# Performance work log

Hardware: AMD Instinct MI355X
Metric: run time of the kernel (lower is better)

## Reference

```python
import jax, jax.numpy as jnp
import numpy as np

NEG_SLOPE = 0.01  # torch F.leaky_relu default
N_USER = 100000
N_ITEM = 100000
N_EDGE = 640000
D = 128
N_LAYERS = 3  # 1 input + num_hidden_layers(1) + 1 output layer


def setup_inputs() -> dict:
    key = jax.random.key(0)
    ks = jax.random.split(key, 10)
    scale = 1.0 / np.sqrt(D)
    return {
        "h_user": jax.random.normal(ks[0], (N_USER, D), dtype=jnp.float32),
        "h_item": jax.random.normal(ks[1], (N_ITEM, D), dtype=jnp.float32),
        # W[layer, etype] : etype 0 = user-follows->user, 1 = user-clicks->item, 2 = item-clicked_by->user
        "W": jax.random.normal(ks[2], (N_LAYERS, 3, D, D), dtype=jnp.float32) * scale,
        "b": jnp.zeros((N_LAYERS, 3, D), dtype=jnp.float32),
        "follows_src": jax.random.randint(ks[3], (N_EDGE,), 0, N_USER, dtype=jnp.int32),
        "follows_dst": jax.random.randint(ks[4], (N_EDGE,), 0, N_USER, dtype=jnp.int32),
        "clicks_src": jax.random.randint(ks[5], (N_EDGE,), 0, N_USER, dtype=jnp.int32),
        "clicks_dst": jax.random.randint(ks[6], (N_EDGE,), 0, N_ITEM, dtype=jnp.int32),
        "cb_src": jax.random.randint(ks[7], (N_EDGE,), 0, N_ITEM, dtype=jnp.int32),
        "cb_dst": jax.random.randint(ks[8], (N_EDGE,), 0, N_USER, dtype=jnp.int32),
    }


def _etype_conv(h_src, W, b, src, dst, n_dst):
    """Per-etype Linear on src nodes, copy_u gather, mean-aggregate at dst."""
    Wh = h_src @ W + b                     # [N_src, D] dense transform (once per node)
    msg = Wh[src]                          # [E, D] gather
    s = jax.ops.segment_sum(msg, dst, num_segments=n_dst)
    cnt = jax.ops.segment_sum(jnp.ones((src.shape[0],), dtype=Wh.dtype), dst, num_segments=n_dst)
    return s / jnp.maximum(cnt, 1.0)[:, None]  # mean; isolated nodes -> 0


def _rgcn_forward(h_user, h_item, W, b, follows_src, follows_dst,
                  clicks_src, clicks_dst, cb_src, cb_dst):
    hu, hi = h_user, h_item
    for l in range(N_LAYERS):
        # per-etype mean aggregation, then cross-etype 'sum' (DGL multi_update_all)
        agg_u = (_etype_conv(hu, W[l, 0], b[l, 0], follows_src, follows_dst, N_USER)
                 + _etype_conv(hi, W[l, 2], b[l, 2], cb_src, cb_dst, N_USER))
        agg_i = _etype_conv(hu, W[l, 1], b[l, 1], clicks_src, clicks_dst, N_ITEM)
        hu = jax.nn.leaky_relu(agg_u, NEG_SLOPE)
        hi = jax.nn.leaky_relu(agg_i, NEG_SLOPE)
    return jnp.stack([hu, hi])  # [2, 100000, 128]


def reference(h_user, h_item, W, b, follows_src, follows_dst,
              clicks_src, clicks_dst, cb_src, cb_dst):
    return _rgcn_forward(h_user, h_item, W, b, follows_src, follows_dst,
                         clicks_src, clicks_dst, cb_src, cb_dst)
```

## Files before the change

### kernel.cpp

```cpp
#include <hip/hip_runtime.h>

typedef unsigned char u8;
typedef unsigned short u16;
typedef _Float16 f16;
typedef __attribute__((ext_vector_type(4))) _Float16 f16x4;
typedef __attribute__((ext_vector_type(8))) _Float16 f16x8;
typedef __attribute__((ext_vector_type(4))) float f32x4;

#define D 128
#define PG 4

__global__ __launch_bounds__(256) void k_pre(
    const float* __restrict__ h_user, const float* __restrict__ h_item,
    const float* __restrict__ W,
    const int* __restrict__ fd, const int* __restrict__ cd,
    const int* __restrict__ cbd,
    u16* __restrict__ h_all, u16* __restrict__ Wtg,
    int* __restrict__ cnt, u8* __restrict__ pos,
    int NU, int NI, int nf, int nc, int ncb,
    int nbCnt, int nbCvtU, int nbCvtI) {
  int b = blockIdx.x;
  int T = gridDim.x;
  long before = (long)b * nbCnt / T;
  long after = (long)(b + 1) * nbCnt / T;
  if (after > before) {
    int e = (int)before * 256 + threadIdx.x;
    int d;
    if (e < nf)
      d = fd[e];
    else if (e < nf + nc)
      d = NU + cd[e - nf];
    else if (e < nf + nc + ncb)
      d = NU + NI + cbd[e - nf - nc];
    else
      return;
    int p = atomicAdd(&cnt[d], 1);
    pos[e] = (u8)p;
  } else {
    int v = b - (int)before;
    if (v < nbCvtU + nbCvtI) {
      bool isU = v < nbCvtU;
      int i = (isU ? v : v - nbCvtU) * 256 + threadIdx.x;
      int n8 = (isU ? NU : NI) * 16;
      if (i >= n8) return;
      const float4* ip = (const float4*)(isU ? h_user : h_item);
      u16* op = h_all + (isU ? 0 : (size_t)NU * D);
      float4 a = ip[i * 2], c = ip[i * 2 + 1];
      f16x8 vv = {(f16)a.x, (f16)a.y, (f16)a.z, (f16)a.w,
                  (f16)c.x, (f16)c.y, (f16)c.z, (f16)c.w};
      *(f16x8*)(op + (size_t)i * 8) = vv;
    } else {
      int idx = (v - nbCvtU - nbCvtI) * 256 + threadIdx.x;
      if (idx >= 9 * 16384) return;
      int mat = idx >> 14;
      int k = (idx >> 7) & 127;
      int n = idx & 127;
      ((f16*)Wtg)[(size_t)mat * 16384 + n * 128 + k] = (f16)W[idx];
    }
  }
}

__device__ __forceinline__ int pad4(int x) { return (x + (PG - 1)) & ~(PG - 1); }

__global__ __launch_bounds__(256) void k_scanA(const int* __restrict__ cnt,
                                               int* __restrict__ part, int n) {
  int t = threadIdx.x;
  int idx = blockIdx.x * 1024 + t * 4;
  int s = 0;
  if (idx + 3 < n) {
    int4 c = *(const int4*)(cnt + idx);
    s = pad4(c.x) + pad4(c.y) + pad4(c.z) + pad4(c.w);
  } else {
#pragma unroll
    for (int j = 0; j < 4; ++j)
      if (idx + j < n) s += pad4(cnt[idx + j]);
  }
  for (int off = 1; off < 64; off <<= 1) s += __shfl_down(s, off, 64);
  __shared__ int ws[4];
  if ((t & 63) == 0) ws[t >> 6] = s;
  __syncthreads();
  if (t == 0) part[blockIdx.x] = ws[0] + ws[1] + ws[2] + ws[3];
}

__global__ __launch_bounds__(1024) void k_scanB(int* __restrict__ part, int n_part) {
  __shared__ int sh[1024];
  int t = threadIdx.x;
  int v = (t < n_part) ? part[t] : 0;
  sh[t] = v;
  __syncthreads();
  for (int off = 1; off < 1024; off <<= 1) {
    int u = (t >= off) ? sh[t - off] : 0;
    __syncthreads();
    sh[t] += u;
    __syncthreads();
  }
  if (t < n_part) part[t] = sh[t] - v;
}

__global__ __launch_bounds__(256) void k_scanC(const int* __restrict__ cnt,
                                               const int* __restrict__ part,
                                               int* __restrict__ rs, int n) {
  int t = threadIdx.x;
  int idx = blockIdx.x * 1024 + t * 4;
  int v0 = 0, v1 = 0, v2 = 0, v3 = 0;
  if (idx + 3 < n) {
    int4 c = *(const int4*)(cnt + idx);
    v0 = pad4(c.x);
    v1 = pad4(c.y);
    v2 = pad4(c.z);
    v3 = pad4(c.w);
  } else {
    if (idx < n) v0 = pad4(cnt[idx]);
    if (idx + 1 < n) v1 = pad4(cnt[idx + 1]);
    if (idx + 2 < n) v2 = pad4(cnt[idx + 2]);
    if (idx + 3 < n) v3 = pad4(cnt[idx + 3]);
  }
  int s = v0 + v1 + v2 + v3;
  int inc = s;
  int lane = t & 63, w = t >> 6;
  for (int off = 1; off < 64; off <<= 1) {
    int u = __shfl_up(inc, off, 64);
    if (lane >= off) inc += u;
  }
  __shared__ int ws[4];
  if (lane == 63) ws[w] = inc;
  __syncthreads();
  int woff = 0;
  for (int i = 0; i < w; ++i) woff += ws[i];
  int ex = part[blockIdx.x] + woff + inc - s;
  int4 r;
  r.x = ex;
  r.y = ex + v0;
  r.z = r.y + v1;
  r.w = r.z + v2;
  if (idx + 3 < n)
    *(int4*)(rs + idx) = r;
  else {
    if (idx < n) rs[idx] = r.x;
    if (idx + 1 < n) rs[idx + 1] = r.y;
    if (idx + 2 < n) rs[idx + 2] = r.z;
    if (idx + 3 < n) rs[idx + 3] = r.w;
  }
  if (idx <= n - 1 && n - 1 < idx + 4) {
    int j = n - 1 - idx;
    int incl = (j == 0) ? r.x + v0 : (j == 1) ? r.y + v1 : (j == 2) ? r.z + v2 : r.w + v3;
    rs[n] = incl;
  }
}

__global__ __launch_bounds__(256) void k_fill2(
    const int* __restrict__ fs, const int* __restrict__ fd,
    const int* __restrict__ cs, const int* __restrict__ cd,
    const int* __restrict__ cbs, const int* __restrict__ cbd,
    const int* __restrict__ rs, const int* __restrict__ cnt,
    const u8* __restrict__ pos, int* __restrict__ csr,
    int NU, int NI, int nf, int nc, int ncb, int nbFill, int N3, int ZR) {
  if ((int)blockIdx.x < nbFill) {
    int e = blockIdx.x * 256 + threadIdx.x;
    int d, s;
    if (e < nf) {
      d = fd[e];
      s = fs[e];
    } else if (e < nf + nc) {
      d = NU + cd[e - nf];
      s = cs[e - nf];
    } else if (e < nf + nc + ncb) {
      d = NU + NI + cbd[e - nf - nc];
      s = cbs[e - nf - nc] + NU;
    } else
      return;
    csr[rs[d] + (int)pos[e]] = s;
  } else {
    int d = (blockIdx.x - nbFill) * 256 + threadIdx.x;
    if (d >= N3) return;
    int deg = cnt[d];
    int degp = pad4(deg);
    int base = rs[d] + deg;
#pragma unroll
    for (int j = 0; j < PG - 1; ++j)
      if (j < degp - deg) csr[base + j] = ZR;
  }
}

__global__ __launch_bounds__(256) void k_agg3(
    const u16* __restrict__ h_all, const int* __restrict__ csr,
    const int* __restrict__ rs, const int* __restrict__ cnt,
    u16* __restrict__ M_all, int N3) {
  int wave = (blockIdx.x * 256 + threadIdx.x) >> 6;
  int lane = threadIdx.x & 63;
  int l16 = lane & 15;
  int w = wave * 4 + (lane >> 4);
  bool valid = w < N3;
  int wc = valid ? w : 0;
  int e = rs[wc];
  int en = valid ? rs[wc + 1] : e;
  int deg = valid ? cnt[wc] : 0;
  f16x8 acc0 = {0, 0, 0, 0, 0, 0, 0, 0};
  f16x8 acc1 = {0, 0, 0, 0, 0, 0, 0, 0};
  const char* hb = (const char*)h_all;
  const int4* csr4 = (const int4*)csr;
  unsigned loff = (unsigned)l16 * 16u;

  int en8 = e + ((en - e) & ~7);
  while (e < en8) {
    int4 c0 = csr4[e >> 2];
    int4 c1 = csr4[(e >> 2) + 1];
    f16x8 v0 = *(const f16x8*)(hb + ((unsigned)c0.x * 256u + loff));
    f16x8 v1 = *(const f16x8*)(hb + ((unsigned)c0.y * 256u + loff));
    f16x8 v2 = *(const f16x8*)(hb + ((unsigned)c0.z * 256u + loff));
    f16x8 v3 = *(const f16x8*)(hb + ((unsigned)c0.w * 256u + loff));
    f16x8 v4 = *(const f16x8*)(hb + ((unsigned)c1.x * 256u + loff));
    f16x8 v5 = *(const f16x8*)(hb + ((unsigned)c1.y * 256u + loff));
    f16x8 v6 = *(const f16x8*)(hb + ((unsigned)c1.z * 256u + loff));
    f16x8 v7 = *(const f16x8*)(hb + ((unsigned)c1.w * 256u + loff));
    acc0 += v0;
    acc1 += v1;
    acc0 += v2;
    acc1 += v3;
    acc0 += v4;
    acc1 += v5;
    acc0 += v6;
    acc1 += v7;
    e += 8;
  }
  if (e < en) {
    int4 c0 = csr4[e >> 2];
    f16x8 v0 = *(const f16x8*)(hb + ((unsigned)c0.x * 256u + loff));
    f16x8 v1 = *(const f16x8*)(hb + ((unsigned)c0.y * 256u + loff));
    f16x8 v2 = *(const f16x8*)(hb + ((unsigned)c0.z * 256u + loff));
    f16x8 v3 = *(const f16x8*)(hb + ((unsigned)c0.w * 256u + loff));
    acc0 += v0;
    acc1 += v1;
    acc0 += v2;
    acc1 += v3;
  }

  if (valid) {
    float invf = deg > 0 ? 1.0f / (float)deg : 0.f;
    f16 hinv = (f16)invf;
    f16x8 t = acc0 + acc1;
    f16x8 r = t * hinv;
    *(f16x8*)((char*)M_all + ((unsigned)wc * 256u + loff)) = r;
  }
}

template <int NE, int OUTF32>
__device__ __forceinline__ void gemm_body(
    const u16* __restrict__ mA, const u16* __restrict__ mBp,
    const u16* __restrict__ wtA, const u16* __restrict__ wtB,
    const float* __restrict__ bA, const float* __restrict__ bB,
    const int* __restrict__ cntA, const int* __restrict__ cntB,
    u16* __restrict__ o16, float* __restrict__ o32, int M, int blk) {
  int tid = threadIdx.x, lane = tid & 63, w = tid >> 6;
  int lr = lane & 15;
  int lk = (lane >> 4) * 8;
  long row0 = (long)blk * 128 + w * 32;

  f32x4 acc[2][8];
#pragma unroll
  for (int rt = 0; rt < 2; rt++)
#pragma unroll
    for (int n = 0; n < 8; n++) acc[rt][n] = (f32x4){0.f, 0.f, 0.f, 0.f};

#pragma unroll
  for (int e = 0; e < NE; ++e) {
    const f16* mm = (const f16*)((e == 0) ? mA : mBp);
    const f16* Wg = (const f16*)((e == 0) ? wtA : wtB);
#pragma unroll
    for (int ks = 0; ks < 4; ++ks) {
      int k0 = ks * 32 + lk;
      f16x8 bf[8];
#pragma unroll
      for (int n = 0; n < 8; n++) bf[n] = *(const f16x8*)(Wg + (n * 16 + lr) * D + k0);
#pragma unroll
      for (int rt = 0; rt < 2; rt++) {
        long r = row0 + rt * 16 + lr;
        if (r >= M) r = M - 1;
        f16x8 af = *(const f16x8*)(mm + r * D + k0);
#pragma unroll
        for (int n = 0; n < 8; n++)
          acc[rt][n] = __builtin_amdgcn_mfma_f32_16x16x32_f16(bf[n], af, acc[rt][n], 0, 0, 0);
      }
    }
  }

  int g4 = (lane >> 4) * 4;
  float4 bAr[8], bBr[8];
#pragma unroll
  for (int n = 0; n < 8; n++) {
    bAr[n] = *(const float4*)&bA[n * 16 + g4];
    if (NE == 2) bBr[n] = *(const float4*)&bB[n * 16 + g4];
  }

#pragma unroll
  for (int rt = 0; rt < 2; rt++) {
    long r = row0 + rt * 16 + lr;
    if (r < M) {
      bool mAok = cntA[r] > 0;
      bool mBok = (NE == 2) && (cntB[r] > 0);
#pragma unroll
      for (int n = 0; n < 8; n++) {
        float4 vv;
        vv.x = acc[rt][n][0];
        vv.y = acc[rt][n][1];
        vv.z = acc[rt][n][2];
        vv.w = acc[rt][n][3];
        if (mAok) {
          vv.x += bAr[n].x;
          vv.y += bAr[n].y;
          vv.z += bAr[n].z;
          vv.w += bAr[n].w;
        }
        if (mBok) {
          vv.x += bBr[n].x;
          vv.y += bBr[n].y;
          vv.z += bBr[n].z;
          vv.w += bBr[n].w;
        }
        vv.x = vv.x > 0.f ? vv.x : 0.01f * vv.x;
        vv.y = vv.y > 0.f ? vv.y : 0.01f * vv.y;
        vv.z = vv.z > 0.f ? vv.z : 0.01f * vv.z;
        vv.w = vv.w > 0.f ? vv.w : 0.01f * vv.w;
        int col = n * 16 + g4;
        if (OUTF32) {
          *(float4*)&o32[r * D + col] = vv;
        } else {
          f16x4 h = {(f16)vv.x, (f16)vv.y, (f16)vv.z, (f16)vv.w};
          *(f16x4*)((f16*)o16 + r * D + col) = h;
        }
      }
    }
  }
}

template <int OUTF32>
__global__ __launch_bounds__(256) void k_gemm2(
    const u16* __restrict__ M_all, const u16* __restrict__ Wl,
    const float* __restrict__ bl, const int* __restrict__ cnt,
    u16* __restrict__ h_all, float* __restrict__ out,
    int NU, int NI, int nbI) {
  if ((int)blockIdx.x < nbI) {
    gemm_body<1, OUTF32>(M_all + (size_t)NU * D, nullptr,
                         Wl + 16384, nullptr,
                         bl + D, nullptr,
                         cnt + NU, nullptr,
                         h_all + (size_t)NU * D, out + (size_t)NU * D, NI,
                         blockIdx.x);
  } else {
    gemm_body<2, OUTF32>(M_all, M_all + (size_t)(NU + NI) * D,
                         Wl, Wl + 2 * 16384,
                         bl, bl + 2 * D,
                         cnt, cnt + NU + NI,
                         h_all, out, NU, blockIdx.x - nbI);
  }
}

extern "C" void kernel_launch(void* const* d_in, const int* in_sizes, int n_in,
                              void* d_out, int out_size, void* d_ws, size_t ws_size,
                              hipStream_t stream) {
  const float* h_user = (const float*)d_in[0];
  const float* h_item = (const float*)d_in[1];
  const float* W = (const float*)d_in[2];
  const float* bb = (const float*)d_in[3];
  const int* f_src = (const int*)d_in[4];
  const int* f_dst = (const int*)d_in[5];
  const int* c_src = (const int*)d_in[6];
  const int* c_dst = (const int*)d_in[7];
  const int* cb_src = (const int*)d_in[8];
  const int* cb_dst = (const int*)d_in[9];

  const int NU = in_sizes[0] / D;
  const int NI = in_sizes[1] / D;
  const int nEf = in_sizes[4], nEc = in_sizes[6], nEcb = in_sizes[8];
  const int N3 = NU + NI + NU;
  const int nE = nEf + nEc + nEcb;
  const int ZR = NU + NI;

  char* p = (char*)d_ws;
  auto alloc = [&](size_t bytes) {
    char* r = p;
    p += (bytes + 255) & ~(size_t)255;
    return r;
  };
  int* cnt = (int*)alloc((size_t)N3 * 4);
  int* rs_all = (int*)alloc((size_t)(N3 + 1) * 4);
  int* part = (int*)alloc(1024 * 4);
  u16* Wtg = (u16*)alloc((size_t)9 * 16384 * 2);
  int* csr_all = (int*)alloc(((size_t)nE + (size_t)(PG - 1) * N3) * 4);
  u16* h_all = (u16*)alloc((size_t)(NU + NI + 1) * D * 2);
  u16* M_all = (u16*)alloc((size_t)N3 * D * 2);
  u8* pos = (u8*)M_all;
  (void)ws_size;

  hipMemsetAsync(cnt, 0, (size_t)N3 * 4, stream);
  hipMemsetAsync(h_all + (size_t)ZR * D, 0, D * 2, stream);

  int nbCnt = (nE + 255) / 256;
  int nbCvtU = (NU * 16 + 255) / 256;
  int nbCvtI = (NI * 16 + 255) / 256;
  int nbW = (9 * 16384 + 255) / 256;
  k_pre<<<nbCnt + nbCvtU + nbCvtI + nbW, 256, 0, stream>>>(
      h_user, h_item, W, f_dst, c_dst, cb_dst, h_all, Wtg, cnt, pos,
      NU, NI, nEf, nEc, nEcb, nbCnt, nbCvtU, nbCvtI);

  int n_part = (N3 + 1023) / 1024;
  k_scanA<<<n_part, 256, 0, stream>>>(cnt, part, N3);
  k_scanB<<<1, 1024, 0, stream>>>(part, n_part);
  k_scanC<<<n_part, 256, 0, stream>>>(cnt, part, rs_all, N3);

  int nbFill = (nE + 255) / 256;
  int nbPad = (N3 + 255) / 256;
  k_fill2<<<nbFill + nbPad, 256, 0, stream>>>(f_src, f_dst, c_src, c_dst,
                                              cb_src, cb_dst, rs_all, cnt, pos,
                                              csr_all, NU, NI, nEf, nEc, nEcb,
                                              nbFill, N3, ZR);

  int nbI = (NI + 127) / 128;
  int nbU = (NU + 127) / 128;
  int agg_blocks = ((N3 + 3) / 4 + 3) / 4;

  for (int l = 0; l < 3; ++l) {
    const u16* Wl = Wtg + (size_t)l * 3 * 16384;
    const float* bl = bb + (size_t)l * 3 * D;

    k_agg3<<<agg_blocks, 256, 0, stream>>>(h_all, csr_all, rs_all, cnt, M_all, N3);

    if (l < 2)
      k_gemm2<0><<<nbI + nbU, 256, 0, stream>>>(M_all, Wl, bl, cnt, h_all,
                                                (float*)d_out, NU, NI, nbI);
    else
      k_gemm2<1><<<nbI + nbU, 256, 0, stream>>>(M_all, Wl, bl, cnt, h_all,
                                                (float*)d_out, NU, NI, nbI);
  }
}
```

Before: 541.5 us.

## Co-schedule aggregation and GEMM blocks in mixed kernels with double-buffered features

Merges the gather/mean aggregation and the MFMA transform into one kernel template, so a single launch runs GEMM blocks for one node type alongside aggregation blocks for the next stage. User and item features are double-buffered and the aggregation buffer is split into three slots, which lets the cross-layer dependencies be staggered. The GEMM tile also shrinks from 128 to 64 rows per block. The aim is to fill the device with independent gather and GEMM work and cut the idle gaps between dependent launches. The cost is more launches, more workspace, and a fallback path when the workspace is too small.

```diff
diff --git a/kernel.cpp b/kernel.cpp
--- a/kernel.cpp
+++ b/kernel.cpp
@@ -182,22 +182,114 @@
   }
 }
 
-__global__ __launch_bounds__(256) void k_agg3(
-    const u16* __restrict__ h_all, const int* __restrict__ csr,
+template <int NE, int OUTF32>
+__device__ __forceinline__ void gemm16(
+    const u16* __restrict__ mA, const u16* __restrict__ mB2,
+    const u16* __restrict__ wA, const u16* __restrict__ wB,
+    const float* __restrict__ bA, const float* __restrict__ bB,
+    const int* __restrict__ cA, const int* __restrict__ cB,
+    u16* __restrict__ ho, float* __restrict__ fo, int M, int blk) {
+  int tid = threadIdx.x, lane = tid & 63;
+  int lr = lane & 15, lk = (lane >> 4) * 8, g4 = (lane >> 4) * 4;
+  int row = blk * 64 + (tid >> 6) * 16 + lr;
+  int rowc = row < M ? row : M - 1;
+  f32x4 acc[8];
+#pragma unroll
+  for (int n = 0; n < 8; ++n) acc[n] = (f32x4){0.f, 0.f, 0.f, 0.f};
+
+#pragma unroll
+  for (int e = 0; e < NE; ++e) {
+    const f16* mm = (const f16*)((e == 0) ? mA : mB2);
+    const f16* Wg = (const f16*)((e == 0) ? wA : wB);
+#pragma unroll
+    for (int ks = 0; ks < 4; ++ks) {
+      f16x8 af = *(const f16x8*)(mm + (size_t)rowc * D + ks * 32 + lk);
+#pragma unroll
+      for (int n = 0; n < 8; ++n) {
+        f16x8 bf = *(const f16x8*)(Wg + (n * 16 + lr) * D + ks * 32 + lk);
+        acc[n] = __builtin_amdgcn_mfma_f32_16x16x32_f16(bf, af, acc[n], 0, 0, 0);
+      }
+    }
+  }
+
+  if (row < M) {
+    bool mAok = cA[row] > 0;
+    bool mBok = (NE == 2) && (cB[row] > 0);
+#pragma unroll
+    for (int n = 0; n < 8; ++n) {
+      int col = n * 16 + g4;
+      float4 vv;
+      vv.x = acc[n][0];
+      vv.y = acc[n][1];
+      vv.z = acc[n][2];
+      vv.w = acc[n][3];
+      if (mAok) {
+        float4 ba = *(const float4*)&bA[col];
+        vv.x += ba.x;
+        vv.y += ba.y;
+        vv.z += ba.z;
+        vv.w += ba.w;
+      }
+      if (mBok) {
+        float4 bbv = *(const float4*)&bB[col];
+        vv.x += bbv.x;
+        vv.y += bbv.y;
+        vv.z += bbv.z;
+        vv.w += bbv.w;
+      }
+      vv.x = vv.x > 0.f ? vv.x : 0.01f * vv.x;
+      vv.y = vv.y > 0.f ? vv.y : 0.01f * vv.y;
+      vv.z = vv.z > 0.f ? vv.z : 0.01f * vv.z;
+      vv.w = vv.w > 0.f ? vv.w : 0.01f * vv.w;
+      if (OUTF32) {
+        *(float4*)&fo[(size_t)row * D + col] = vv;
+      } else {
+        f16x4 h = {(f16)vv.x, (f16)vv.y, (f16)vv.z, (f16)vv.w};
+        *(f16x4*)((f16*)ho + (size_t)row * D + col) = h;
+      }
+    }
+  }
+}
+
+template <int OUTF32, int GR>
+__global__ __launch_bounds__(256) void k_mix(
+    const u16* __restrict__ hagg, const int* __restrict__ csr,
     const int* __restrict__ rs, const int* __restrict__ cnt,
-    u16* __restrict__ M_all, int N3) {
-  int wave = (blockIdx.x * 256 + threadIdx.x) >> 6;
+    u16* __restrict__ M_all,
+    const u16* __restrict__ Mrd, const u16* __restrict__ Mrd2,
+    const u16* __restrict__ wA, const u16* __restrict__ wB,
+    const float* __restrict__ bA, const float* __restrict__ bB,
+    const int* __restrict__ cA, const int* __restrict__ cB,
+    u16* __restrict__ ho, float* __restrict__ fo, int Mrows, int nbG,
+    int b1, int n1, int m1, int b2, int n2, int m2) {
+  int b = blockIdx.x;
+  long bef = 0, aft = 0;
+  if (GR) {
+    int T = gridDim.x;
+    bef = (long)b * nbG / T;
+    aft = (long)(b + 1) * nbG / T;
+  }
+  if (GR && aft > bef) {
+    gemm16<(GR == 2 ? 2 : 1), OUTF32>(Mrd, Mrd2, wA, wB, bA, bB, cA, cB,
+                                      ho, fo, Mrows, (int)bef);
+    return;
+  }
+  int ab = b - (int)bef;
+  int wave = ab * 4 + ((int)threadIdx.x >> 6);
   int lane = threadIdx.x & 63;
   int l16 = lane & 15;
   int w = wave * 4 + (lane >> 4);
-  bool valid = w < N3;
+  int ntot = n1 + n2;
+  bool valid = w < ntot;
   int wc = valid ? w : 0;
-  int e = rs[wc];
-  int en = valid ? rs[wc + 1] : e;
-  int deg = valid ? cnt[wc] : 0;
+  int node = wc < n1 ? b1 + wc : b2 + (wc - n1);
+  int mrow = wc < n1 ? m1 + wc : m2 + (wc - n1);
+  int e = rs[node];
+  int en = valid ? rs[node + 1] : e;
+  int deg = valid ? cnt[node] : 0;
   f16x8 acc0 = {0, 0, 0, 0, 0, 0, 0, 0};
   f16x8 acc1 = {0, 0, 0, 0, 0, 0, 0, 0};
-  const char* hb = (const char*)h_all;
+  const char* hb = (const char*)hagg;
   const int4* csr4 = (const int4*)csr;
   unsigned loff = (unsigned)l16 * 16u;
 
@@ -240,118 +332,7 @@
     f16 hinv = (f16)invf;
     f16x8 t = acc0 + acc1;
     f16x8 r = t * hinv;
-    *(f16x8*)((char*)M_all + ((unsigned)wc * 256u + loff)) = r;
-  }
-}
-
-template <int NE, int OUTF32>
-__device__ __forceinline__ void gemm_body(
-    const u16* __restrict__ mA, const u16* __restrict__ mBp,
-    const u16* __restrict__ wtA, const u16* __restrict__ wtB,
-    const float* __restrict__ bA, const float* __restrict__ bB,
-    const int* __restrict__ cntA, const int* __restrict__ cntB,
-    u16* __restrict__ o16, float* __restrict__ o32, int M, int blk) {
-  int tid = threadIdx.x, lane = tid & 63, w = tid >> 6;
-  int lr = lane & 15;
-  int lk = (lane >> 4) * 8;
-  long row0 = (long)blk * 128 + w * 32;
-
-  f32x4 acc[2][8];
-#pragma unroll
-  for (int rt = 0; rt < 2; rt++)
-#pragma unroll
-    for (int n = 0; n < 8; n++) acc[rt][n] = (f32x4){0.f, 0.f, 0.f, 0.f};
-
-#pragma unroll
-  for (int e = 0; e < NE; ++e) {
-    const f16* mm = (const f16*)((e == 0) ? mA : mBp);
-    const f16* Wg = (const f16*)((e == 0) ? wtA : wtB);
-#pragma unroll
-    for (int ks = 0; ks < 4; ++ks) {
-      int k0 = ks * 32 + lk;
-      f16x8 bf[8];
-#pragma unroll
-      for (int n = 0; n < 8; n++) bf[n] = *(const f16x8*)(Wg + (n * 16 + lr) * D + k0);
-#pragma unroll
-      for (int rt = 0; rt < 2; rt++) {
-        long r = row0 + rt * 16 + lr;
-        if (r >= M) r = M - 1;
-        f16x8 af = *(const f16x8*)(mm + r * D + k0);
-#pragma unroll
-        for (int n = 0; n < 8; n++)
-          acc[rt][n] = __builtin_amdgcn_mfma_f32_16x16x32_f16(bf[n], af, acc[rt][n], 0, 0, 0);
-      }
-    }
-  }
-
-  int g4 = (lane >> 4) * 4;
-  float4 bAr[8], bBr[8];
-#pragma unroll
-  for (int n = 0; n < 8; n++) {
-    bAr[n] = *(const float4*)&bA[n * 16 + g4];
-    if (NE == 2) bBr[n] = *(const float4*)&bB[n * 16 + g4];
-  }
-
-#pragma unroll
-  for (int rt = 0; rt < 2; rt++) {
-    long r = row0 + rt * 16 + lr;
-    if (r < M) {
-      bool mAok = cntA[r] > 0;
-      bool mBok = (NE == 2) && (cntB[r] > 0);
-#pragma unroll
-      for (int n = 0; n < 8; n++) {
-        float4 vv;
-        vv.x = acc[rt][n][0];
-        vv.y = acc[rt][n][1];
-        vv.z = acc[rt][n][2];
-        vv.w = acc[rt][n][3];
-        if (mAok) {
-          vv.x += bAr[n].x;
-          vv.y += bAr[n].y;
-          vv.z += bAr[n].z;
-          vv.w += bAr[n].w;
-        }
-        if (mBok) {
-          vv.x += bBr[n].x;
-          vv.y += bBr[n].y;
-          vv.z += bBr[n].z;
-          vv.w += bBr[n].w;
-        }
-        vv.x = vv.x > 0.f ? vv.x : 0.01f * vv.x;
-        vv.y = vv.y > 0.f ? vv.y : 0.01f * vv.y;
-        vv.z = vv.z > 0.f ? vv.z : 0.01f * vv.z;
-        vv.w = vv.w > 0.f ? vv.w : 0.01f * vv.w;
-        int col = n * 16 + g4;
-        if (OUTF32) {
-          *(float4*)&o32[r * D + col] = vv;
-        } else {
-          f16x4 h = {(f16)vv.x, (f16)vv.y, (f16)vv.z, (f16)vv.w};
-          *(f16x4*)((f16*)o16 + r * D + col) = h;
-        }
-      }
-    }
-  }
-}
-
-template <int OUTF32>
-__global__ __launch_bounds__(256) void k_gemm2(
-    const u16* __restrict__ M_all, const u16* __restrict__ Wl,
-    const float* __restrict__ bl, const int* __restrict__ cnt,
-    u16* __restrict__ h_all, float* __restrict__ out,
-    int NU, int NI, int nbI) {
-  if ((int)blockIdx.x < nbI) {
-    gemm_body<1, OUTF32>(M_all + (size_t)NU * D, nullptr,
-                         Wl + 16384, nullptr,
-                         bl + D, nullptr,
-                         cnt + NU, nullptr,
-                         h_all + (size_t)NU * D, out + (size_t)NU * D, NI,
-                         blockIdx.x);
-  } else {
-    gemm_body<2, OUTF32>(M_all, M_all + (size_t)(NU + NI) * D,
-                         Wl, Wl + 2 * 16384,
-                         bl, bl + 2 * D,
-                         cnt, cnt + NU + NI,
-                         h_all, out, NU, blockIdx.x - nbI);
+    *(f16x8*)((char*)M_all + ((size_t)mrow * 256u + loff)) = r;
   }
 }
 
@@ -375,6 +356,14 @@
   const int N3 = NU + NI + NU;
   const int nE = nEf + nEc + nEcb;
   const int ZR = NU + NI;
+  const int NM = (NU > NI ? NU : NI);
+
+  size_t fixedB = ((size_t)N3 * 4 + 255 + (size_t)(N3 + 1) * 4 + 255 + 4096 + 255 +
+                   (size_t)9 * 16384 * 2 + 255 +
+                   ((size_t)nE + (size_t)(PG - 1) * N3) * 4 + 255);
+  size_t hbytes = (size_t)(NU + NI + 1) * D * 2 + 255;
+  size_t needPipe = fixedB + 2 * hbytes + (size_t)3 * NM * D * 2 + 1024;
+  bool pipe = needPipe <= ws_size;
 
   char* p = (char*)d_ws;
   auto alloc = [&](size_t bytes) {
@@ -384,23 +373,24 @@
   };
   int* cnt = (int*)alloc((size_t)N3 * 4);
   int* rs_all = (int*)alloc((size_t)(N3 + 1) * 4);
-  int* part = (int*)alloc(1024 * 4);
+  int* part = (int*)alloc(4096);
   u16* Wtg = (u16*)alloc((size_t)9 * 16384 * 2);
   int* csr_all = (int*)alloc(((size_t)nE + (size_t)(PG - 1) * N3) * 4);
-  u16* h_all = (u16*)alloc((size_t)(NU + NI + 1) * D * 2);
-  u16* M_all = (u16*)alloc((size_t)N3 * D * 2);
+  u16* hA = (u16*)alloc(hbytes);
+  u16* hB = pipe ? (u16*)alloc(hbytes) : hA;
+  u16* M_all = (u16*)alloc(pipe ? (size_t)3 * NM * D * 2 : (size_t)N3 * D * 2);
   u8* pos = (u8*)M_all;
-  (void)ws_size;
 
   hipMemsetAsync(cnt, 0, (size_t)N3 * 4, stream);
-  hipMemsetAsync(h_all + (size_t)ZR * D, 0, D * 2, stream);
+  hipMemsetAsync(hA + (size_t)ZR * D, 0, D * 2, stream);
+  if (pipe) hipMemsetAsync(hB + (size_t)ZR * D, 0, D * 2, stream);
 
   int nbCnt = (nE + 255) / 256;
   int nbCvtU = (NU * 16 + 255) / 256;
   int nbCvtI = (NI * 16 + 255) / 256;
   int nbW = (9 * 16384 + 255) / 256;
   k_pre<<<nbCnt + nbCvtU + nbCvtI + nbW, 256, 0, stream>>>(
-      h_user, h_item, W, f_dst, c_dst, cb_dst, h_all, Wtg, cnt, pos,
+      h_user, h_item, W, f_dst, c_dst, cb_dst, hA, Wtg, cnt, pos,
       NU, NI, nEf, nEc, nEcb, nbCnt, nbCvtU, nbCvtI);
 
   int n_part = (N3 + 1023) / 1024;
@@ -415,21 +405,86 @@
                                               csr_all, NU, NI, nEf, nEc, nEcb,
                                               nbFill, N3, ZR);
 
-  int nbI = (NI + 127) / 128;
-  int nbU = (NU + 127) / 128;
-  int agg_blocks = ((N3 + 3) / 4 + 3) / 4;
-
-  for (int l = 0; l < 3; ++l) {
-    const u16* Wl = Wtg + (size_t)l * 3 * 16384;
-    const float* bl = bb + (size_t)l * 3 * D;
-
-    k_agg3<<<agg_blocks, 256, 0, stream>>>(h_all, csr_all, rs_all, cnt, M_all, N3);
-
-    if (l < 2)
-      k_gemm2<0><<<nbI + nbU, 256, 0, stream>>>(M_all, Wl, bl, cnt, h_all,
-                                                (float*)d_out, NU, NI, nbI);
-    else
-      k_gemm2<1><<<nbI + nbU, 256, 0, stream>>>(M_all, Wl, bl, cnt, h_all,
-                                                (float*)d_out, NU, NI, nbI);
-  }
-}
+  float* out_u = (float*)d_out;
+  float* out_i = (float*)d_out + (size_t)NU * D;
+  auto aggB = [](int n) { return (n + 15) / 16; };
+
+  if (pipe) {
+    const int S1 = 0, S2 = NM, S3 = 2 * NM;
+    int nbI = (NI + 63) / 64, nbU = (NU + 63) / 64;
+    const u16 *Wl0 = Wtg, *Wl1 = Wtg + 3 * 16384, *Wl2 = Wtg + 6 * 16384;
+    const float *bl0 = bb, *bl1 = bb + 3 * D, *bl2 = bb + 6 * D;
+
+    k_mix<0, 0><<<aggB(NI), 256, 0, stream>>>(
+        hA, csr_all, rs_all, cnt, M_all, nullptr, nullptr, nullptr, nullptr,
+        nullptr, nullptr, nullptr, nullptr, nullptr, nullptr, 0, 0,
+        NU, NI, S2, 0, 0, 0);
+    k_mix<0, 1><<<nbI + aggB(2 * NU), 256, 0, stream>>>(
+        hA, csr_all, rs_all, cnt, M_all, M_all + (size_t)S2 * D, nullptr,
+        Wl0 + 16384, nullptr, bl0 + D, nullptr, cnt + NU, nullptr,
+        hB + (size_t)NU * D, nullptr, NI, nbI,
+        0, NU, S1, NU + NI, NU, S3);
+    k_mix<0, 2><<<nbU + aggB(NU), 256, 0, stream>>>(
+        hB, csr_all, rs_all, cnt, M_all, M_all + (size_t)S1 * D,
+        M_all + (size_t)S3 * D, Wl0, Wl0 + 2 * 16384, bl0, bl0 + 2 * D,
+        cnt, cnt + NU + NI, hB, nullptr, NU, nbU,
+        NU + NI, NU, S2, 0, 0, 0);
+    k_mix<0, 0><<<aggB(NI), 256, 0, stream>>>(
+        hB, csr_all, rs_all, cnt, M_all, nullptr, nullptr, nullptr, nullptr,
+        nullptr, nullptr, nullptr, nullptr, nullptr, nullptr, 0, 0,
+        NU, NI, S3, 0, 0, 0);
+    k_mix<0, 1><<<nbI + aggB(NU), 256, 0, stream>>>(
+        hB, csr_all, rs_all, cnt, M_all, M_all + (size_t)S3 * D, nullptr,
+        Wl1 + 16384, nullptr, bl1 + D, nullptr, cnt + NU, nullptr,
+        hA + (size_t)NU * D, nullptr, NI, nbI,
+        0, NU, S1, 0, 0, 0);
+    k_mix<0, 2><<<nbU + aggB(NU), 256, 0, stream>>>(
+        hA, csr_all, rs_all, cnt, M_all, M_all + (size_t)S1 * D,
+        M_all + (size_t)S2 * D, Wl1, Wl1 + 2 * 16384, bl1, bl1 + 2 * D,
+        cnt, cnt + NU + NI, hA, nullptr, NU, nbU,
+        NU + NI, NU, S3, 0, 0, 0);
+    k_mix<0, 0><<<aggB(NI), 256, 0, stream>>>(
+        hA, csr_all, rs_all, cnt, M_all, nullptr, nullptr, nullptr, nullptr,
+        nullptr, nullptr, nullptr, nullptr, nullptr, nullptr, 0, 0,
+        NU, NI, S2, 0, 0, 0);
+    k_mix<1, 1><<<nbI + aggB(NU), 256, 0, stream>>>(
+        hA, csr_all, rs_all, cnt, M_all, M_all + (size_t)S2 * D, nullptr,
+        Wl2 + 16384, nullptr, bl2 + D, nullptr, cnt + NU, nullptr,
+        nullptr, out_i, NI, nbI,
+        0, NU, S1, 0, 0, 0);
+    k_mix<1, 2><<<nbU, 256, 0, stream>>>(
+        hA, csr_all, rs_all, cnt, M_all, M_all + (size_t)S1 * D,
+        M_all + (size_t)S3 * D, Wl2, Wl2 + 2 * 16384, bl2, bl2 + 2 * D,
+        cnt, cnt + NU + NI, nullptr, out_u, NU, nbU,
+        0, 0, 0, 0, 0, 0);
+  } else {
+    int nbI = (NI + 63) / 64, nbU = (NU + 63) / 64;
+    for (int l = 0; l < 3; ++l) {
+      const u16* Wl = Wtg + (size_t)l * 3 * 16384;
+      const float* bl = bb + (size_t)l * 3 * D;
+      k_mix<0, 0><<<aggB(N3), 256, 0, stream>>>(
+          hA, csr_all, rs_all, cnt, M_all, nullptr, nullptr, nullptr, nullptr,
+          nullptr, nullptr, nullptr, nullptr, nullptr, nullptr, 0, 0,
+          0, N3, 0, 0, 0, 0);
+      if (l < 2) {
+        k_mix<0, 1><<<nbI, 256, 0, stream>>>(
+            hA, csr_all, rs_all, cnt, M_all, M_all + (size_t)NU * D, nullptr,
+            Wl + 16384, nullptr, bl + D, nullptr, cnt + NU, nullptr,
+            hA + (size_t)NU * D, nullptr, NI, nbI, 0, 0, 0, 0, 0, 0);
+        k_mix<0, 2><<<nbU, 256, 0, stream>>>(
+            hA, csr_all, rs_all, cnt, M_all, M_all,
+            M_all + (size_t)(NU + NI) * D, Wl, Wl + 2 * 16384, bl, bl + 2 * D,
+            cnt, cnt + NU + NI, hA, nullptr, NU, nbU, 0, 0, 0, 0, 0, 0);
+      } else {
+        k_mix<1, 1><<<nbI, 256, 0, stream>>>(
+            hA, csr_all, rs_all, cnt, M_all, M_all + (size_t)NU * D, nullptr,
+            Wl + 16384, nullptr, bl + D, nullptr, cnt + NU, nullptr,
+            nullptr, out_i, NI, nbI, 0, 0, 0, 0, 0, 0);
+        k_mix<1, 2><<<nbU, 256, 0, stream>>>(
+            hA, csr_all, rs_all, cnt, M_all, M_all,
+            M_all + (size_t)(NU + NI) * D, Wl, Wl + 2 * 16384, bl, bl + 2 * D,
+            cnt, cnt + NU + NI, nullptr, out_u, NU, nbU, 0, 0, 0, 0, 0, 0);
+      }
+    }
+  }
+}
```

New measurement: 669.5 us. 1.24x slower.
